# Kernel tuning notes

Measured on AMD Instinct MI355X. Metric: run time of the kernel, lower is better.

The kernel has to match this reference:

```python
import jax, jax.numpy as jnp
import numpy as np

NUM_SAMPLE = 10   # self._num, hard-coded as range(10) in prob_sample
FSCALE = 5        # neighbor-count kernel
CSCALE = 3        # constraint-count kernel
EPS = 1e-16


def _sum_window(x, k):
    # x: [N,H,W] -> SAME-padded k x k box sum == F.conv2d with ones(1,1,k,k), padding=(k-1)//2
    return jax.lax.reduce_window(x, 0.0, jax.lax.add, (1, k, k), (1, 1, 1), 'SAME')


def _dilate8(x):
    # 3x3 max-pool = one step of 8-connectivity dilation (skimage flood_fill default
    # connectivity for 2D is full connectivity when my_connectivity is None)
    return jax.lax.reduce_window(x, 0.0, jax.lax.max, (1, 3, 3), (1, 1, 1), 'SAME')


def _flood_fill(fg, seed_r, seed_c):
    # fg: [N,H,W] binary float; returns the fg-connected component containing the seed,
    # via fixed-point iteration of masked dilation (equivalent to skimage.flood_fill
    # seeded at the max-neighbor pixel, then thresholding the filled value).
    N, H, W = fg.shape
    reach0 = jnp.zeros_like(fg).at[jnp.arange(N), seed_r, seed_c].set(1.0) * fg

    def cond(st):
        _, changed, it = st
        return changed & (it < H * W)

    def body(st):
        reach, _, it = st
        new = jnp.maximum(reach, _dilate8(reach) * fg)
        return new, jnp.any(new > reach), it + 1

    reach, _, _ = jax.lax.while_loop(cond, body, (reach0, jnp.array(True), jnp.int32(0)))
    return reach


def connectivity_rewards(sample_ns, fg_num):
    # sample_ns: [n, S, H, W] int class indices. Returns binary rewards [n, S, H, W]
    # (reward_type='binary', run_state='train'). All (image, sample) pairs processed
    # in one batched flood fill per foreground class.
    n, S, H, W = sample_ns.shape
    flat = sample_ns.reshape(n * S, H, W)
    total = jnp.zeros((n * S, H, W), jnp.float32)
    for class_idx in range(1, fg_num):  # small fixed loop over fg classes
        fg = (flat == class_idx).astype(jnp.float32)
        neigh = _sum_window(fg, FSCALE) * fg           # count_neighbor * fg
        neigh_flat = neigh.reshape(n * S, H * W)
        seed = jnp.argmax(neigh_flat, axis=-1)          # pixel with max neighbor count
        has_fg = (jnp.max(neigh_flat, axis=-1) > 0).astype(jnp.float32)
        fill = _flood_fill(fg, seed // W, seed % W) * has_fg[:, None, None]
        Fc = _sum_window(fill, CSCALE) * fill           # F_fg_neigbors
        Sc = _sum_window(fg, CSCALE) * fg               # S_fg_neigbors
        r = (jnp.where(Fc == 0, -1.0, Fc) == jnp.where(Sc == 0, -2.0, Sc)).astype(jnp.float32)
        total = total + r
    return total.reshape(n, S, H, W)


def setup_inputs() -> dict:
    key = jax.random.key(0)
    logits = jax.random.normal(key, (4, 4, 512, 512), dtype=jnp.float32)
    preds = jax.nn.softmax(logits, axis=1)  # per-pixel class probabilities [n,c,h,w]
    return {"preds": preds}


def reference(preds):
    n, c, h, w = preds.shape
    skey = jax.random.key(42)
    # prob_sample: per-pixel multinomial over classes, repeated NUM_SAMPLE times
    lg = jnp.moveaxis(jnp.log(preds + EPS), 1, -1)  # [n,h,w,c]
    samp = jax.random.categorical(skey, lg, axis=-1, shape=(NUM_SAMPLE, n, h, w))
    sample_ns = jnp.transpose(samp, (1, 0, 2, 3)).astype(jnp.int32)  # [n,S,h,w]
    prob_ns = jnp.take_along_axis(preds, sample_ns, axis=1)          # [n,S,h,w]
    rewards = jax.lax.stop_gradient(connectivity_rewards(sample_ns, c))
    # REINFORCE objective: maximize reward-weighted log-prob of sampled labelings
    loss = -(rewards * jnp.log(prob_ns + EPS)).mean()
    return loss
```

## Files before the change

### kernel.cpp

```cpp
#include <hip/hip_runtime.h>
#include <stdint.h>

#define JAX_PARTITIONABLE 1

#define SNUM 10
#define NBATCH 4
#define NCLS 4
#define HH 512
#define WW 512
#define IMG (HH*WW)
#define NPIX (SNUM*NBATCH*IMG)
#define GUMTOT ((uint32_t)NPIX*NCLS)
#define HALFG (GUMTOT/2u)
#define WPI (IMG/32)
#define QCAP 3584

#if __has_builtin(__builtin_amdgcn_alignbit)
__device__ __forceinline__ uint32_t rotl32(uint32_t x, int r) {
  return __builtin_amdgcn_alignbit(x, x, (uint32_t)(32 - r));
}
#else
__device__ __forceinline__ uint32_t rotl32(uint32_t x, int r) {
  return (x << r) | (x >> (32 - r));
}
#endif

__device__ __forceinline__ void tf2x32(uint32_t x0, uint32_t x1,
                                       uint32_t& o0, uint32_t& o1) {
  const uint32_t k0 = 0u, k1 = 42u;
  const uint32_t k2 = k0 ^ k1 ^ 0x1BD11BDAu;
  x0 += k0; x1 += k1;
#define TFR(r) { x0 += x1; x1 = rotl32(x1, (r)); x1 ^= x0; }
  TFR(13) TFR(15) TFR(26) TFR(6)
  x0 += k1; x1 += k2 + 1u;
  TFR(17) TFR(29) TFR(16) TFR(24)
  x0 += k2; x1 += k0 + 2u;
  TFR(13) TFR(15) TFR(26) TFR(6)
  x0 += k0; x1 += k1 + 3u;
  TFR(17) TFR(29) TFR(16) TFR(24)
  x0 += k1; x1 += k2 + 4u;
  TFR(13) TFR(15) TFR(26) TFR(6)
  x0 += k2; x1 += k0 + 5u;
#undef TFR
  o0 = x0; o1 = x1;
}

__device__ __forceinline__ float u01(uint32_t bits) {
  const float f = __uint_as_float((bits >> 9) | 0x3f800000u) - 1.0f;
  return fmaxf(f, 1.17549435e-38f);
}

__device__ __forceinline__ uint32_t gum_bits(uint32_t g) {
#if JAX_PARTITIONABLE
  uint32_t y0, y1;
  tf2x32(0u, g, y0, y1);
  return y0 ^ y1;
#else
  uint32_t y0, y1;
  uint32_t j = (g < HALFG) ? g : (g - HALFG);
  tf2x32(j, j + HALFG, y0, y1);
  return (g < HALFG) ? y0 : y1;
#endif
}

__device__ __forceinline__ uint32_t unpack32(uint64_t v) {
  uint64_t tt = v | (v >> 1);
  uint64_t u = ~tt & 0x5555555555555555ULL;
  u = (u ^ (u >> 1))  & 0x3333333333333333ULL;
  u = (u ^ (u >> 2))  & 0x0F0F0F0F0F0F0F0FULL;
  u = (u ^ (u >> 4))  & 0x00FF00FF00FF00FFULL;
  u = (u ^ (u >> 8))  & 0x0000FFFF0000FFFFULL;
  u = (u ^ (u >> 16)) & 0x00000000FFFFFFFFULL;
  return (uint32_t)u;
}

__global__ __launch_bounds__(256) void k_sample(const float* __restrict__ preds,
                                                uint8_t* __restrict__ packed,
                                                float* __restrict__ acc,
                                                uint32_t* __restrict__ gkey,
                                                uint32_t* __restrict__ misc) {
  const int t = blockIdx.x * 256 + threadIdx.x;
  if (t == 0) acc[0] = 0.0f;
  if (t < 120) gkey[t] = 0u;
  if (t == 120) misc[0] = 0u;
  const int sn = t >> 16;
  const int n  = sn & 3;
  const int pg = t & 65535;
  const int pix = pg << 2;

  float pp[NCLS][4];
#pragma unroll
  for (int c = 0; c < NCLS; ++c) {
    const float4 v = *reinterpret_cast<const float4*>(
        preds + (((int64_t)(n * NCLS + c)) << 18) + pix);
    pp[c][0] = v.x; pp[c][1] = v.y; pp[c][2] = v.z; pp[c][3] = v.w;
  }

  const uint32_t gb = (uint32_t)sn * 1048576u + ((uint32_t)pix << 2);
  uint32_t byte = 0;
#pragma unroll
  for (int j = 0; j < 4; ++j) {
    float bp = pp[0][j];
    float bl = __log2f(u01(gum_bits(gb + (uint32_t)(j * 4))));
    int bc = 0;
#pragma unroll
    for (int c = 1; c < NCLS; ++c) {
      const float lc = __log2f(u01(gum_bits(gb + (uint32_t)(j * 4 + c))));
      if (pp[c][j] * bl < bp * lc) { bp = pp[c][j]; bl = lc; bc = c; }
    }
    byte |= (uint32_t)bc << (2 * j);
  }
  packed[t] = (uint8_t)byte;
}

__global__ __launch_bounds__(256) void k_argmax(const uint8_t* __restrict__ packed,
                                                uint32_t* __restrict__ gkey) {
  __shared__ uint32_t sfg[36 * 16];
  __shared__ uint32_t skey;
  const int tid = threadIdx.x;
  const int b = blockIdx.x;
  const int prob = b >> 4;
  const int slab = b & 15;
  const int sn = prob % 40;
  const int k  = 1 + prob / 40;
  if (tid == 0) skey = 0u;

  const uint64_t* p64 = reinterpret_cast<const uint64_t*>(packed);
  const uint64_t pat = (uint64_t)k * 0x5555555555555555ULL;
  const int gr0 = slab * 32 - 2;
  for (int wi = tid; wi < 36 * 16; wi += 256) {
    const int gr = gr0 + (wi >> 4);
    uint32_t m = 0;
    if (gr >= 0 && gr < HH)
      m = unpack32(p64[(int64_t)sn * WPI + (gr << 4) + (wi & 15)] ^ pat);
    sfg[wi] = m;
  }
  __syncthreads();

  uint32_t lbest = 0;
  for (int idx = tid; idx < 512; idx += 256) {
    const int rl = 2 + (idx >> 4);
    const int col = idx & 15;
    const uint32_t cw = sfg[(rl << 4) + col];
    if (!cw) continue;
    uint64_t rb[5];
#pragma unroll
    for (int d = 0; d < 5; ++d) {
      const int base = ((rl + d - 2) << 4) + col;
      const uint32_t le = (col > 0)  ? sfg[base - 1] : 0u;
      const uint32_t cu = sfg[base];
      const uint32_t ri = (col < 15) ? sfg[base + 1] : 0u;
      rb[d] = ((uint64_t)(ri & 7u) << 34) | ((uint64_t)cu << 2) | (uint64_t)(le >> 30);
    }
    const int gr = slab * 32 + (idx >> 4);
    uint32_t bits = cw;
    while (bits) {
      const int j = __ffs(bits) - 1;
      bits &= bits - 1;
      int cnt = 0;
#pragma unroll
      for (int d = 0; d < 5; ++d)
        cnt += __popc((uint32_t)(rb[d] >> j) & 0x1fu);
      const uint32_t fidx = (uint32_t)((gr << 9) + (col << 5) + j);
      const uint32_t key = ((uint32_t)cnt << 18) | (0x3FFFFu - fidx);
      lbest = lbest > key ? lbest : key;
    }
  }
#pragma unroll
  for (int off = 32; off > 0; off >>= 1) {
    const uint32_t o = (uint32_t)__shfl_down((int)lbest, off, 64);
    lbest = lbest > o ? lbest : o;
  }
  if ((threadIdx.x & 63) == 0 && lbest) atomicMax(&skey, lbest);
  __syncthreads();
  if (tid == 0 && skey) atomicMax(&gkey[prob], skey);
}


__device__ __forceinline__ uint32_t runmask(uint32_t m, uint32_t s) {
  uint32_t out = 0;
  while (s) {
    const int j = __ffs(s) - 1;
    const uint32_t bj = 1u << j;
    const uint32_t up = ((m + bj) ^ m) & m;
    const uint32_t rm = __brev(m);
    const uint32_t rbj = 1u << (31 - j);
    const uint32_t dn = __brev(((rm + rbj) ^ rm) & rm);
    const uint32_t run = up | dn;
    out |= run;
    s &= ~run;
  }
  return out;
}

__device__ __forceinline__ void claimf(uint32_t* fg, uint32_t* qw, uint32_t* qb,
                                       uint32_t* qtail, uint32_t t, uint32_t want) {
  const uint32_t old = atomicAnd(&fg[t], ~want);
  uint32_t nb = old & want;
  if (!nb) return;
  const uint32_t ext = runmask(old, nb) & ~nb;
  if (ext) {
    const uint32_t old2 = atomicAnd(&fg[t], ~ext);
    nb |= old2 & ext;
  }
  const uint32_t slot = atomicAdd(qtail, 1u);
  if (slot < QCAP) { qw[slot] = t; qb[slot] = nb; }
}

__device__ __forceinline__ uint64_t shup64(uint64_t v) {
  const uint32_t lo = __shfl_up((unsigned int)v, 1, 64);
  const uint32_t hi = __shfl_up((unsigned int)(v >> 32), 1, 64);
  return ((uint64_t)hi << 32) | lo;
}
__device__ __forceinline__ uint64_t shdn64(uint64_t v) {
  const uint32_t lo = __shfl_down((unsigned int)v, 1, 64);
  const uint32_t hi = __shfl_down((unsigned int)(v >> 32), 1, 64);
  return ((uint64_t)hi << 32) | lo;
}

__global__ __launch_bounds__(64) void k_fill(const float* __restrict__ preds,
                                             const uint8_t* __restrict__ packed,
                                             const uint32_t* __restrict__ gkey,
                                             uint32_t* __restrict__ misc,
                                             float* __restrict__ acc,
                                             float* __restrict__ out) {
  __shared__ uint32_t fg[WPI];
  __shared__ uint32_t qw[QCAP];
  __shared__ uint32_t qb[QCAP];
  __shared__ uint32_t qtail;
  const int tid = threadIdx.x;
  const int prob = blockIdx.x;
  const int sn = prob % 40;
  const int k  = 1 + prob / 40;
  const int n  = sn & 3;
  uint32_t* filldone = misc + 0;

  const uint32_t bkey = gkey[prob];
  float local = 0.0f;
  if ((bkey >> 18) != 0u) {
    const uint32_t seed = 0x3FFFFu - (bkey & 0x3FFFFu);
    const int sr = (int)(seed >> 9), sc = (int)(seed & 511);
    const float* chan = preds + (((int64_t)n) * NCLS + k) * (int64_t)IMG;
    const uint64_t* p64 = reinterpret_cast<const uint64_t*>(packed);
    const uint64_t pat = (uint64_t)k * 0x5555555555555555ULL;

    int r0 = sr - 31; if (r0 < 0) r0 = 0; if (r0 > HH - 64) r0 = HH - 64;
    int cl = (sc >> 5) - (((sc & 31) < 16) ? 1 : 0);
    if (cl < 0) cl = 0; if (cl > 14) cl = 14;
    const int ar = r0 + tid;
    const int64_t pb = (int64_t)sn * WPI + (ar << 4) + cl;
    const uint64_t fgw = ((uint64_t)unpack32(p64[pb + 1] ^ pat) << 32)
                       |            unpack32(p64[pb]     ^ pat);
    uint64_t fill = (ar == sr) ? (1ULL << (sc - (cl << 5))) : 0ULL;

    bool conv = false;
    for (int it = 0; it < 2048; ++it) {
      uint64_t up = shup64(fill); if (tid == 0)  up = 0ULL;
      uint64_t dn = shdn64(fill); if (tid == 63) dn = 0ULL;
      const uint64_t sp = fill | up | dn;
      const uint64_t nf = (fgw & (sp | (sp << 1) | (sp >> 1))) | fill;
      const bool ch = (nf != fill);
      fill = nf;
      if (__ballot(ch) == 0ULL) { conv = true; break; }
    }

    bool esc = !conv;
    if (fill) {
      if (tid == 0 && r0 > 0) esc = true;
      if (tid == 63 && r0 + 63 < HH - 1) esc = true;
      if ((fill & 1ULL) && cl > 0) esc = true;
      if ((fill >> 63) && cl < 14) esc = true;
    }

    if (__ballot(esc) == 0ULL) {
      uint64_t bits = fill;
      const float* rowp = chan + (int64_t)ar * WW + (cl << 5);
      while (bits) {
        const int j = __ffsll((unsigned long long)bits) - 1;
        bits &= bits - 1;
        local += logf(rowp[j] + 1e-16f);
      }
    } else {
      if (tid == 0) qtail = 0u;
      for (int wi = tid; wi < WPI; wi += 64)
        fg[wi] = unpack32(p64[(int64_t)sn * WPI + wi] ^ pat);
      __syncthreads();
      claimf(fg, qw, qb, &qtail, seed >> 5, 1u << (seed & 31));
      uint32_t head = 0;
      while (true) {
        uint32_t tail = atomicAdd(&qtail, 0u);
        if (tail > QCAP) tail = QCAP;
        if (head >= tail) break;
        for (uint32_t i = head + (uint32_t)tid; i < tail; i += 64) {
          const uint32_t w = qw[i], got = qb[i];
          const int row = (int)(w >> 4), cb = (int)(w & 15);
          const uint32_t spread = got | (got << 1) | (got >> 1);
          const bool lo = (got & 1u) != 0u, hi = (got >> 31) != 0u;
          if (row > 0) {
            claimf(fg, qw, qb, &qtail, w - 16, spread);
            if (cb > 0 && lo)  claimf(fg, qw, qb, &qtail, w - 17, 0x80000000u);
            if (cb < 15 && hi) claimf(fg, qw, qb, &qtail, w - 15, 1u);
          }
          if (row < HH - 1) {
            claimf(fg, qw, qb, &qtail, w + 16, spread);
            if (cb > 0 && lo)  claimf(fg, qw, qb, &qtail, w + 15, 0x80000000u);
            if (cb < 15 && hi) claimf(fg, qw, qb, &qtail, w + 17, 1u);
          }
          if (cb > 0 && lo)  claimf(fg, qw, qb, &qtail, w - 1, 0x80000000u);
          if (cb < 15 && hi) claimf(fg, qw, qb, &qtail, w + 1, 1u);
        }
        head = tail;
      }
      uint32_t tot = qtail; if (tot > QCAP) tot = QCAP;
      for (uint32_t i = (uint32_t)tid; i < tot; i += 64) {
        const uint32_t w = qw[i];
        uint32_t bits = qb[i];
        const int row = (int)(w >> 4);
        const int colb = (int)(w & 15) << 5;
        const float* rowp = chan + (int64_t)row * WW;
        while (bits) {
          const int j = __ffs(bits) - 1;
          bits &= bits - 1;
          local += logf(rowp[colb + j] + 1e-16f);
        }
      }
    }
  }

#pragma unroll
  for (int off = 32; off > 0; off >>= 1)
    local += __shfl_down(local, off, 64);
  if (tid == 0) {
    if (local != 0.0f) atomicAdd(acc, local);
    __threadfence();
    const uint32_t old = atomicAdd(filldone, 1u);
    if (old == 119u) {
      const float s = atomicAdd(acc, 0.0f);
      out[0] = -s / 10485760.0f;
    }
  }
}

extern "C" void kernel_launch(void* const* d_in, const int* in_sizes, int n_in,
                              void* d_out, int out_size, void* d_ws, size_t ws_size,
                              hipStream_t stream) {
  const float* preds = (const float*)d_in[0];
  float* out = (float*)d_out;
  char* ws = (char*)d_ws;
  float*    acc    = (float*)ws;
  uint32_t* gkey   = (uint32_t*)(ws + 64);
  uint32_t* misc   = (uint32_t*)(ws + 1536);
  uint8_t*  packed = (uint8_t*)(ws + 4096);

  k_sample<<<10240, 256, 0, stream>>>(preds, packed, acc, gkey, misc);
  k_argmax<<<1920, 256, 0, stream>>>(packed, gkey);
  k_fill<<<120, 64, 0, stream>>>(preds, packed, gkey, misc, acc, out);
}
```

Measured before the change: 159.9 us.

## Interleave Threefry across classes, use run-based horizontal fill, widen fill fallback block

The sampling kernel now computes the four per-class Threefry hashes side by side in arrays so their independent rounds can interleave for ILP, and the non-partitionable code path is dropped. The local flood fill extends whole contiguous foreground runs within each 64-bit row segment per iteration, using add-carry tricks on the forward and bit-reversed masks, which is meant to cut the number of wavefront iterations. The global BFS fallback runs with 256 threads and barrier-synchronised queue tails instead of one wave polling atomics, with a cross-wave reduction added at the end. The extra barriers and the per-iteration run loop add overhead in exchange.

```diff
diff --git a/kernel.cpp b/kernel.cpp
--- a/kernel.cpp
+++ b/kernel.cpp
@@ -1,7 +1,5 @@
 #include <hip/hip_runtime.h>
 #include <stdint.h>
-
-#define JAX_PARTITIONABLE 1
 
 #define SNUM 10
 #define NBATCH 4
@@ -10,57 +8,12 @@
 #define WW 512
 #define IMG (HH*WW)
 #define NPIX (SNUM*NBATCH*IMG)
-#define GUMTOT ((uint32_t)NPIX*NCLS)
-#define HALFG (GUMTOT/2u)
 #define WPI (IMG/32)
 #define QCAP 3584
-
-#if __has_builtin(__builtin_amdgcn_alignbit)
-__device__ __forceinline__ uint32_t rotl32(uint32_t x, int r) {
-  return __builtin_amdgcn_alignbit(x, x, (uint32_t)(32 - r));
-}
-#else
-__device__ __forceinline__ uint32_t rotl32(uint32_t x, int r) {
-  return (x << r) | (x >> (32 - r));
-}
-#endif
-
-__device__ __forceinline__ void tf2x32(uint32_t x0, uint32_t x1,
-                                       uint32_t& o0, uint32_t& o1) {
-  const uint32_t k0 = 0u, k1 = 42u;
-  const uint32_t k2 = k0 ^ k1 ^ 0x1BD11BDAu;
-  x0 += k0; x1 += k1;
-#define TFR(r) { x0 += x1; x1 = rotl32(x1, (r)); x1 ^= x0; }
-  TFR(13) TFR(15) TFR(26) TFR(6)
-  x0 += k1; x1 += k2 + 1u;
-  TFR(17) TFR(29) TFR(16) TFR(24)
-  x0 += k2; x1 += k0 + 2u;
-  TFR(13) TFR(15) TFR(26) TFR(6)
-  x0 += k0; x1 += k1 + 3u;
-  TFR(17) TFR(29) TFR(16) TFR(24)
-  x0 += k1; x1 += k2 + 4u;
-  TFR(13) TFR(15) TFR(26) TFR(6)
-  x0 += k2; x1 += k0 + 5u;
-#undef TFR
-  o0 = x0; o1 = x1;
-}
 
 __device__ __forceinline__ float u01(uint32_t bits) {
   const float f = __uint_as_float((bits >> 9) | 0x3f800000u) - 1.0f;
   return fmaxf(f, 1.17549435e-38f);
-}
-
-__device__ __forceinline__ uint32_t gum_bits(uint32_t g) {
-#if JAX_PARTITIONABLE
-  uint32_t y0, y1;
-  tf2x32(0u, g, y0, y1);
-  return y0 ^ y1;
-#else
-  uint32_t y0, y1;
-  uint32_t j = (g < HALFG) ? g : (g - HALFG);
-  tf2x32(j, j + HALFG, y0, y1);
-  return (g < HALFG) ? y0 : y1;
-#endif
 }
 
 __device__ __forceinline__ uint32_t unpack32(uint64_t v) {
@@ -97,19 +50,54 @@
   }
 
   const uint32_t gb = (uint32_t)sn * 1048576u + ((uint32_t)pix << 2);
+  const uint32_t k1 = 42u;
+  const uint32_t k2 = 42u ^ 0x1BD11BDAu;
   uint32_t byte = 0;
+
+#define TFR4(r) { \
+  _Pragma("unroll") \
+  for (int c_ = 0; c_ < 4; ++c_) { \
+    x0[c_] += x1[c_]; \
+    const uint32_t xr_ = x1[c_]; \
+    x1[c_] = ((xr_ << (r)) | (xr_ >> (32 - (r)))) ^ x0[c_]; \
+  } }
+#define INJ4(a, b) { \
+  _Pragma("unroll") \
+  for (int c_ = 0; c_ < 4; ++c_) { x0[c_] += (a); x1[c_] += (b); } }
+
 #pragma unroll
   for (int j = 0; j < 4; ++j) {
+    uint32_t x0[4], x1[4];
+#pragma unroll
+    for (int c = 0; c < 4; ++c) {
+      x0[c] = 0u;
+      x1[c] = gb + (uint32_t)(4 * j + c) + k1;
+    }
+    TFR4(13) TFR4(15) TFR4(26) TFR4(6)
+    INJ4(k1, k2 + 1u)
+    TFR4(17) TFR4(29) TFR4(16) TFR4(24)
+    INJ4(k2, 2u)
+    TFR4(13) TFR4(15) TFR4(26) TFR4(6)
+    INJ4(0u, k1 + 3u)
+    TFR4(17) TFR4(29) TFR4(16) TFR4(24)
+    INJ4(k1, k2 + 4u)
+    TFR4(13) TFR4(15) TFR4(26) TFR4(6)
+    float lg[4];
+#pragma unroll
+    for (int c = 0; c < 4; ++c)
+      lg[c] = __log2f(u01((x0[c] + k2) ^ (x1[c] + 5u)));
+
     float bp = pp[0][j];
-    float bl = __log2f(u01(gum_bits(gb + (uint32_t)(j * 4))));
+    float bl = lg[0];
     int bc = 0;
 #pragma unroll
     for (int c = 1; c < NCLS; ++c) {
-      const float lc = __log2f(u01(gum_bits(gb + (uint32_t)(j * 4 + c))));
-      if (pp[c][j] * bl < bp * lc) { bp = pp[c][j]; bl = lc; bc = c; }
+      if (pp[c][j] * bl < bp * lg[c]) { bp = pp[c][j]; bl = lg[c]; bc = c; }
     }
     byte |= (uint32_t)bc << (2 * j);
   }
+#undef TFR4
+#undef INJ4
   packed[t] = (uint8_t)byte;
 }
 
@@ -218,16 +206,19 @@
   return ((uint64_t)hi << 32) | lo;
 }
 
-__global__ __launch_bounds__(64) void k_fill(const float* __restrict__ preds,
-                                             const uint8_t* __restrict__ packed,
-                                             const uint32_t* __restrict__ gkey,
-                                             uint32_t* __restrict__ misc,
-                                             float* __restrict__ acc,
-                                             float* __restrict__ out) {
+__global__ __launch_bounds__(256) void k_fill(const float* __restrict__ preds,
+                                              const uint8_t* __restrict__ packed,
+                                              const uint32_t* __restrict__ gkey,
+                                              uint32_t* __restrict__ misc,
+                                              float* __restrict__ acc,
+                                              float* __restrict__ out) {
   __shared__ uint32_t fg[WPI];
   __shared__ uint32_t qw[QCAP];
   __shared__ uint32_t qb[QCAP];
   __shared__ uint32_t qtail;
+  __shared__ uint32_t sfb;
+  __shared__ uint32_t stail;
+  __shared__ float    sred[4];
   const int tid = threadIdx.x;
   const int prob = blockIdx.x;
   const int sn = prob % 40;
@@ -235,63 +226,84 @@
   const int n  = sn & 3;
   uint32_t* filldone = misc + 0;
 
+  if (tid == 0) { sfb = 0u; qtail = 0u; }
+  __syncthreads();
+
   const uint32_t bkey = gkey[prob];
+  const uint32_t seed = 0x3FFFFu - (bkey & 0x3FFFFu);
+  const float* chan = preds + (((int64_t)n) * NCLS + k) * (int64_t)IMG;
+  const uint64_t* p64 = reinterpret_cast<const uint64_t*>(packed);
+  const uint64_t pat = (uint64_t)k * 0x5555555555555555ULL;
   float local = 0.0f;
+
   if ((bkey >> 18) != 0u) {
-    const uint32_t seed = 0x3FFFFu - (bkey & 0x3FFFFu);
-    const int sr = (int)(seed >> 9), sc = (int)(seed & 511);
-    const float* chan = preds + (((int64_t)n) * NCLS + k) * (int64_t)IMG;
-    const uint64_t* p64 = reinterpret_cast<const uint64_t*>(packed);
-    const uint64_t pat = (uint64_t)k * 0x5555555555555555ULL;
-
-    int r0 = sr - 31; if (r0 < 0) r0 = 0; if (r0 > HH - 64) r0 = HH - 64;
-    int cl = (sc >> 5) - (((sc & 31) < 16) ? 1 : 0);
-    if (cl < 0) cl = 0; if (cl > 14) cl = 14;
-    const int ar = r0 + tid;
-    const int64_t pb = (int64_t)sn * WPI + (ar << 4) + cl;
-    const uint64_t fgw = ((uint64_t)unpack32(p64[pb + 1] ^ pat) << 32)
-                       |            unpack32(p64[pb]     ^ pat);
-    uint64_t fill = (ar == sr) ? (1ULL << (sc - (cl << 5))) : 0ULL;
-
-    bool conv = false;
-    for (int it = 0; it < 2048; ++it) {
-      uint64_t up = shup64(fill); if (tid == 0)  up = 0ULL;
-      uint64_t dn = shdn64(fill); if (tid == 63) dn = 0ULL;
-      const uint64_t sp = fill | up | dn;
-      const uint64_t nf = (fgw & (sp | (sp << 1) | (sp >> 1))) | fill;
-      const bool ch = (nf != fill);
-      fill = nf;
-      if (__ballot(ch) == 0ULL) { conv = true; break; }
-    }
-
-    bool esc = !conv;
-    if (fill) {
-      if (tid == 0 && r0 > 0) esc = true;
-      if (tid == 63 && r0 + 63 < HH - 1) esc = true;
-      if ((fill & 1ULL) && cl > 0) esc = true;
-      if ((fill >> 63) && cl < 14) esc = true;
-    }
-
-    if (__ballot(esc) == 0ULL) {
-      uint64_t bits = fill;
-      const float* rowp = chan + (int64_t)ar * WW + (cl << 5);
-      while (bits) {
-        const int j = __ffsll((unsigned long long)bits) - 1;
-        bits &= bits - 1;
-        local += logf(rowp[j] + 1e-16f);
-      }
-    } else {
-      if (tid == 0) qtail = 0u;
-      for (int wi = tid; wi < WPI; wi += 64)
+    if (tid < 64) {
+      const int sr = (int)(seed >> 9), sc = (int)(seed & 511);
+      int r0 = sr - 31; if (r0 < 0) r0 = 0; if (r0 > HH - 64) r0 = HH - 64;
+      int cl = (sc >> 5) - (((sc & 31) < 16) ? 1 : 0);
+      if (cl < 0) cl = 0; if (cl > 14) cl = 14;
+      const int ar = r0 + tid;
+      const int64_t pb = (int64_t)sn * WPI + (ar << 4) + cl;
+      const uint64_t fgw = ((uint64_t)unpack32(p64[pb + 1] ^ pat) << 32)
+                         |            unpack32(p64[pb]     ^ pat);
+      const uint64_t rfg = __brevll(fgw);
+      uint64_t fill = (ar == sr) ? (1ULL << (sc - (cl << 5))) : 0ULL;
+
+      bool conv = false;
+      for (int it = 0; it < 2048; ++it) {
+        uint64_t up = shup64(fill); if (tid == 0)  up = 0ULL;
+        uint64_t dn = shdn64(fill); if (tid == 63) dn = 0ULL;
+        const uint64_t sp = fill | up | dn;
+        uint64_t s = fgw & (sp | (sp << 1) | (sp >> 1));
+        uint64_t nf = 0ULL;
+        while (s) {
+          const int j = __ffsll((unsigned long long)s) - 1;
+          const uint64_t upr = ((fgw + (1ULL << j)) ^ fgw) & fgw;
+          const uint64_t dnr = __brevll(((rfg + (1ULL << (63 - j))) ^ rfg) & rfg);
+          const uint64_t run = upr | dnr;
+          nf |= run;
+          s &= ~run;
+        }
+        const bool ch = (nf != fill);
+        fill = nf;
+        if (__ballot(ch) == 0ULL) { conv = true; break; }
+      }
+
+      bool esc = !conv;
+      if (fill) {
+        if (tid == 0 && r0 > 0) esc = true;
+        if (tid == 63 && r0 + 63 < HH - 1) esc = true;
+        if ((fill & 1ULL) && cl > 0) esc = true;
+        if ((fill >> 63) && cl < 14) esc = true;
+      }
+
+      if (__ballot(esc) == 0ULL) {
+        uint64_t bits = fill;
+        const float* rowp = chan + (int64_t)ar * WW + (cl << 5);
+        while (bits) {
+          const int j = __ffsll((unsigned long long)bits) - 1;
+          bits &= bits - 1;
+          local += logf(rowp[j] + 1e-16f);
+        }
+      } else if (tid == 0) {
+        sfb = 1u;
+      }
+    }
+    __syncthreads();
+
+    if (sfb) {
+      for (int wi = tid; wi < WPI; wi += 256)
         fg[wi] = unpack32(p64[(int64_t)sn * WPI + wi] ^ pat);
       __syncthreads();
       claimf(fg, qw, qb, &qtail, seed >> 5, 1u << (seed & 31));
       uint32_t head = 0;
       while (true) {
-        uint32_t tail = atomicAdd(&qtail, 0u);
-        if (tail > QCAP) tail = QCAP;
+        __syncthreads();
+        if (tid == 0) { uint32_t tl = qtail; stail = tl > QCAP ? QCAP : tl; }
+        __syncthreads();
+        const uint32_t tail = stail;
         if (head >= tail) break;
-        for (uint32_t i = head + (uint32_t)tid; i < tail; i += 64) {
+        for (uint32_t i = head + (uint32_t)tid; i < tail; i += 256) {
           const uint32_t w = qw[i], got = qb[i];
           const int row = (int)(w >> 4), cb = (int)(w & 15);
           const uint32_t spread = got | (got << 1) | (got >> 1);
@@ -311,8 +323,8 @@
         }
         head = tail;
       }
-      uint32_t tot = qtail; if (tot > QCAP) tot = QCAP;
-      for (uint32_t i = (uint32_t)tid; i < tot; i += 64) {
+      const uint32_t tot = stail;
+      for (uint32_t i = (uint32_t)tid; i < tot; i += 256) {
         const uint32_t w = qw[i];
         uint32_t bits = qb[i];
         const int row = (int)(w >> 4);
@@ -330,8 +342,11 @@
 #pragma unroll
   for (int off = 32; off > 0; off >>= 1)
     local += __shfl_down(local, off, 64);
+  if ((tid & 63) == 0) sred[tid >> 6] = local;
+  __syncthreads();
   if (tid == 0) {
-    if (local != 0.0f) atomicAdd(acc, local);
+    const float tot = sred[0] + sred[1] + sred[2] + sred[3];
+    if (tot != 0.0f) atomicAdd(acc, tot);
     __threadfence();
     const uint32_t old = atomicAdd(filldone, 1u);
     if (old == 119u) {
@@ -354,5 +369,5 @@
 
   k_sample<<<10240, 256, 0, stream>>>(preds, packed, acc, gkey, misc);
   k_argmax<<<1920, 256, 0, stream>>>(packed, gkey);
-  k_fill<<<120, 64, 0, stream>>>(preds, packed, gkey, misc, acc, out);
-}
+  k_fill<<<120, 256, 0, stream>>>(preds, packed, gkey, misc, acc, out);
+}
```

Measured after the change: 163.0 us. Within noise of the previous version (+1.9%).
